# Performance work log

Measured on AMD Instinct MI355X. Metric: run time of the kernel, lower is better.

Reference implementation:

```python
import jax, jax.numpy as jnp
import numpy as np

N, E = 8000, 64000
DNE, DED, DXPD = 128, 128, 64
H, LMAX = 8, 2
S = 1 + 2 * LMAX            # 5 coefficient slots
CD = S * DNE                # coeff_dim = 640
DH = DNE // H               # head dim = 16
CH = CD // H                # coeff head = 80


def _lin(k, din, dout):
    # xavier-ish init for a [din, dout] weight used as x @ W
    return (jax.random.normal(k, (din, dout), jnp.float32) / np.sqrt(din)).astype(jnp.float32)


def _mlp(x, W1, b1, W2, b2):
    # Linear -> SiLU -> (Dropout p, eval) -> Linear
    return jax.nn.silu(x @ W1 + b1) @ W2 + b2


def _seg_sum(x, idx, n):
    return jax.ops.segment_sum(x, idx, num_segments=n)


def _rej(x, r):
    # vector_rejection: remove component of x [E,m,d] parallel to r [E,m]
    r3 = r[:, :, None]
    return x - jnp.sum(x * r3, axis=1, keepdims=True) * r3


def setup_inputs() -> dict:
    key = jax.random.key(0)
    ks = jax.random.split(key, 40)
    inp = {
        "h":  jax.random.normal(ks[0], (N, DNE), jnp.float32),
        "t":  jax.random.normal(ks[1], (E, DED), jnp.float32),
        "X1": jax.random.normal(ks[2], (N, 3, DNE), jnp.float32),
        "X2": jax.random.normal(ks[3], (N, 5, DNE), jnp.float32),
        "r1": jax.random.normal(ks[4], (E, 3), jnp.float32),
        "r2": jax.random.normal(ks[5], (E, 5), jnp.float32),
        "c":  jax.random.uniform(ks[6], (E, 1), jnp.float32),
        "edge": jax.random.randint(ks[7], (E, 2), 0, N, jnp.int32),
    }
    # GATA params
    inp["Wq"], inp["bq"] = _lin(ks[8], DNE, DNE), jnp.zeros((DNE,), jnp.float32)
    inp["Wk"], inp["bk"] = _lin(ks[9], DNE, DNE), jnp.zeros((DNE,), jnp.float32)
    inp["Wre"], inp["bre"] = _lin(ks[10], DED, DNE), jnp.zeros((DNE,), jnp.float32)
    inp["Wv1"], inp["bv1"] = _lin(ks[11], DNE, DNE), jnp.zeros((DNE,), jnp.float32)
    inp["Wv2"], inp["bv2"] = _lin(ks[12], DNE, CD), jnp.zeros((CD,), jnp.float32)
    inp["Wrs"], inp["brs"] = _lin(ks[13], DED, CD), jnp.zeros((CD,), jnp.float32)
    inp["Ws1"], inp["bs1"] = _lin(ks[14], DNE, DNE), jnp.zeros((DNE,), jnp.float32)
    inp["Ws2"], inp["bs2"] = _lin(ks[15], DNE, CD), jnp.zeros((CD,), jnp.float32)
    # HTR params
    inp["Wvq"] = _lin(ks[16], DNE, DXPD)
    inp["Wvk1"] = _lin(ks[17], DNE, DXPD)
    inp["Wvk2"] = _lin(ks[18], DNE, DXPD)
    inp["Ww1"], inp["bw1"] = _lin(ks[19], DXPD, DXPD), jnp.zeros((DXPD,), jnp.float32)
    inp["Ww2"], inp["bw2"] = _lin(ks[20], DXPD, DED), jnp.zeros((DED,), jnp.float32)
    inp["Wt1"], inp["bt1"] = _lin(ks[21], DED, DED), jnp.zeros((DED,), jnp.float32)
    inp["Wt2"], inp["bt2"] = _lin(ks[22], DED, DED), jnp.zeros((DED,), jnp.float32)
    return inp


def reference(h, t, X1, X2, r1, r2, c, edge,
              Wq, bq, Wk, bk, Wre, bre, Wv1, bv1, Wv2, bv2,
              Wrs, brs, Ws1, bs1, Ws2, bs2,
              Wvq, Wvk1, Wvk2, Ww1, bw1, Ww2, bw2, Wt1, bt1, Wt2, bt2):
    i, j = edge[:, 0], edge[:, 1]
    # multi-head attention logits over edges
    q = (h[i] @ Wq + bq).reshape(E, H, DH)
    k = (h[j] @ Wk + bk).reshape(E, H, DH)
    geom = jax.nn.silu(t @ Wre + bre).reshape(E, H, DH)
    alpha = jnp.sum(q * (k * geom), axis=-1)                       # [E,H]
    # segment softmax over destination node i
    mx = jnp.full((N, H), -jnp.inf, jnp.float32).at[i].max(alpha)
    mx = jnp.maximum(mx, -1e9)
    ex = jnp.exp(alpha - mx[i])
    den = jnp.maximum(_seg_sum(ex, i, N), 1e-12)
    attn = ex / den[i]
    deg = jnp.zeros((N,), jnp.float32).at[i].add(1.0)              # bincount
    attn = attn * (jnp.sqrt(deg[i]) / np.sqrt(DNE))[:, None]       # [E,H]
    # values + spatial branch
    v = _mlp(h[j], Wv1, bv1, Wv2, bv2).reshape(E, H, CH)
    sea = attn[:, :, None] * v
    tp = (t @ Wrs + brs).reshape(E, H, CH)
    s = _mlp(h[j], Ws1, bs1, Ws2, bs2).reshape(E, H, CH)
    spatial = tp * s * c[:, None, :]
    coeff = (sea + spatial).reshape(E, S, DNE)
    # scalar update
    h_out = h + _seg_sum(coeff[:, 0, :], i, N)
    # steerable updates (l = 1, 2)
    Xl, rl, X_out = [X1, X2], [r1, r2], []
    for l in (1, 2):
        o_d = coeff[:, l, :]          # direction coeff
        o_t = coeff[:, LMAX + l, :]   # tensor coeff
        msg = rl[l - 1][:, :, None] * o_d[:, None, :] + Xl[l - 1][j] * o_t[:, None, :]
        X_out.append(Xl[l - 1] + _seg_sum(msg, i, N))
    # HTR edge refinement
    Xcat = jnp.concatenate(X_out, axis=1)                          # [N,8,dne]
    Q = (Xcat @ Wvq)[i]                                            # [E,8,dxpd]
    K = jnp.concatenate([X_out[0] @ Wvk1, X_out[1] @ Wvk2], axis=1)[j]
    Q = jnp.concatenate([_rej(Q[:, :3], r1), _rej(Q[:, 3:], r2)], axis=1)
    K = jnp.concatenate([_rej(K[:, :3], -r1), _rej(K[:, 3:], -r2)], axis=1)
    w = jnp.sum(Q * K, axis=1)                                     # [E,dxpd]
    t_out = t + _mlp(w, Ww1, bw1, Ww2, bw2) * _mlp(t, Wt1, bt1, Wt2, bt2)
    return (h_out, t_out, X_out[0], X_out[1])
```

## Files before the change

kernel.cpp:

```cpp
#include <hip/hip_runtime.h>
#include <cstdint>
#include <cmath>

#define NN 8000
#define NE 64000
#define DNE 128
#define NHD 8
#define CDIM 640

typedef unsigned short u16;
typedef u16   u16x8 __attribute__((ext_vector_type(8)));
typedef __bf16 v8bf __attribute__((ext_vector_type(8)));
typedef float  v4f  __attribute__((ext_vector_type(4)));

static __device__ __forceinline__ u16 f2bf(float f) {
    unsigned int u = __float_as_uint(f);
    u += 0x7FFF + ((u >> 16) & 1);
    return (u16)(u >> 16);
}
static __device__ __forceinline__ float bf2f(u16 v) {
    return __uint_as_float(((unsigned int)v) << 16);
}

constexpr size_t O_TBF   = 0;
constexpr size_t O_X1BF  = O_TBF   + 16384000;
constexpr size_t O_X2BF  = O_X1BF  + 6160384;
constexpr size_t O_X1OBF = O_X2BF  + 10256384;
constexpr size_t O_X2OBF = O_X1OBF + 6160384;
constexpr size_t O_WARE  = O_X2OBF + 10256384;
constexpr size_t O_CNT   = O_WARE  + 811008;
constexpr size_t O_CURS  = O_CNT   + 32000;
constexpr size_t O_OFFS  = O_CURS  + 32000;
constexpr size_t O_EIDS  = O_OFFS  + 32768;
constexpr size_t O_HV    = O_EIDS  + 256000;
constexpr size_t O_HS    = O_HV    + 10321920;
constexpr size_t O_ATTN  = O_HS    + 10321920;
constexpr size_t O_TEMP  = O_ATTN  + 2048000;
constexpr size_t O_GEOM  = O_TEMP;
constexpr size_t O_HQ    = O_GEOM + 16384000;
constexpr size_t O_HK    = O_HQ   + 2064384;
constexpr size_t O_VMID  = O_HK   + 2064384;
constexpr size_t O_SMID  = O_VMID + 2064384;
constexpr size_t O_ALPHA = O_SMID + 2064384;
constexpr size_t O_COEFF = O_TEMP;
constexpr size_t O_Q1K1  = O_TEMP;
constexpr size_t O_Q2K2  = O_Q1K1 + 6160384;
constexpr size_t O_WBUF  = O_Q2K2 + 10256384;
constexpr size_t O_WMID  = O_WBUF + 8192000;
constexpr size_t O_WOUT  = O_WMID + 8192000;
constexpr size_t O_TMID  = O_WOUT + 16384000;

__device__ const int WOFFA[14] = {0,16384,32768,49152,65536,81920,98304,114688,196608,278528,360448,364544,372736,389120};

struct WTArgs { const float* w[16]; };
__global__ void wtrans_all(WTArgs a, u16* __restrict__ ob) {
    int s = blockIdx.y;
    int id = blockIdx.x * 256 + threadIdx.x;
    if (s < 12) {
        int K = (s < 10) ? 128 : 64;
        int N = (s < 7) ? 128 : ((s < 10) ? 640 : ((s == 10) ? 64 : 128));
        if (id >= K * N) return;
        int k = id / N, n = id % N;
        ob[WOFFA[s] + (size_t)n * K + k] = f2bf(a.w[s][id]);
    } else {
        if (id >= 16384) return;
        int n = id >> 7, k = id & 127;
        const float* wa = a.w[s == 12 ? 12 : 14];
        const float* wb = a.w[s == 12 ? 13 : 15];
        ob[WOFFA[s] + id] = f2bf(n < 64 ? wa[k * 64 + n] : wb[k * 64 + (n - 64)]);
    }
}

struct ConvArgs { const float* in[4]; u16* out[4]; };
__global__ void conv_all(ConvArgs a) {
    int s = blockIdx.y;
    int padr = (s == 0) ? 8064 : ((s == 1) ? 64000 : ((s == 2) ? 24064 : 40064));
    int realr = (s == 0) ? 8000 : ((s == 1) ? 64000 : ((s == 2) ? 24000 : 40000));
    int id4 = (blockIdx.x * 256 + threadIdx.x) * 4;
    if (id4 >= padr * 128) return;
    int row = id4 >> 7;
    float4 v = make_float4(0.f, 0.f, 0.f, 0.f);
    if (row < realr) v = *(const float4*)(a.in[s] + id4);
    u16* o = a.out[s] + id4;
    o[0] = f2bf(v.x); o[1] = f2bf(v.y); o[2] = f2bf(v.z); o[3] = f2bf(v.w);
}

template<int BN, int WROWS, int WCOLS, int MODE>
__global__ __launch_bounds__(256) void mm_bf16(
    const u16* __restrict__ A, const u16* __restrict__ Bt,
    const float* __restrict__ bias, void* __restrict__ out,
    int Ncols, int K, int act,
    const int* __restrict__ edge, const float* __restrict__ attn,
    const u16* __restrict__ hv, const u16* __restrict__ hs,
    const float* __restrict__ cvals,
    const float* __restrict__ tresid, const u16* __restrict__ wmul)
{
    constexpr int BM = 128, BK = 32, LDA = 40;
    constexpr int MT = BM / WROWS / 16;
    constexpr int NT = BN / WCOLS / 16;
    __shared__ u16 sA[BM * LDA];
    __shared__ u16 sB[BN * LDA];
    const int tid = threadIdx.x;
    const int wave = tid >> 6, lane = tid & 63;
    const int lane15 = lane & 15, quad = lane >> 4;
    const int wm = wave / WCOLS, wn = wave % WCOLS;
    const int row0 = blockIdx.y * BM, col0 = blockIdx.x * BN;
    const int arow = wm * (BM / WROWS);
    const int brow = wn * (BN / WCOLS);
    v4f acc[MT][NT] = {};
    for (int k0 = 0; k0 < K; k0 += BK) {
        #pragma unroll
        for (int ci = 0; ci < (BM * BK / 8) / 256; ++ci) {
            int cch = tid + ci * 256;
            int m = cch >> 2, ko = (cch & 3) * 8;
            u16x8 v = *(const u16x8*)(A + (size_t)(row0 + m) * K + k0 + ko);
            *(u16x8*)(&sA[m * LDA + ko]) = v;
        }
        #pragma unroll
        for (int ci = 0; ci < (BN * BK / 8) / 256; ++ci) {
            int cch = tid + ci * 256;
            int n = cch >> 2, ko = (cch & 3) * 8;
            u16x8 v = *(const u16x8*)(Bt + (size_t)(col0 + n) * K + k0 + ko);
            *(u16x8*)(&sB[n * LDA + ko]) = v;
        }
        __syncthreads();
        v8bf af[MT], bfr[NT];
        #pragma unroll
        for (int mt = 0; mt < MT; ++mt)
            af[mt] = __builtin_bit_cast(v8bf, *(const u16x8*)(&sA[(arow + mt * 16 + lane15) * LDA + quad * 8]));
        #pragma unroll
        for (int nt = 0; nt < NT; ++nt)
            bfr[nt] = __builtin_bit_cast(v8bf, *(const u16x8*)(&sB[(brow + nt * 16 + lane15) * LDA + quad * 8]));
        #pragma unroll
        for (int mt = 0; mt < MT; ++mt)
            #pragma unroll
            for (int nt = 0; nt < NT; ++nt)
                acc[mt][nt] = __builtin_amdgcn_mfma_f32_16x16x32_bf16(af[mt], bfr[nt], acc[mt][nt], 0, 0, 0);
        __syncthreads();
    }
    #pragma unroll
    for (int mt = 0; mt < MT; ++mt) {
        #pragma unroll
        for (int r = 0; r < 4; ++r) {
            int grow = row0 + arow + mt * 16 + quad * 4 + r;
            if (MODE == 2) {
                int e = grow;
                int jn = edge[2 * e + 1];
                float ce = cvals[e];
                const u16* hvr = hv + (size_t)jn * CDIM;
                const u16* hsr = hs + (size_t)jn * CDIM;
                u16* orow = (u16*)out + (size_t)e * CDIM;
                #pragma unroll
                for (int nt = 0; nt < NT; ++nt) {
                    int gcol = col0 + brow + nt * 16 + lane15;
                    float tp = acc[mt][nt][r] + bias[gcol];
                    float at = attn[e * NHD + gcol / 80];
                    float v = at * bf2f(hvr[gcol]) + tp * bf2f(hsr[gcol]) * ce;
                    orow[gcol] = f2bf(v);
                }
            } else if (MODE == 3) {
                size_t base = (size_t)grow * Ncols;
                #pragma unroll
                for (int nt = 0; nt < NT; ++nt) {
                    int gcol = col0 + brow + nt * 16 + lane15;
                    float v = acc[mt][nt][r] + bias[gcol];
                    ((float*)out)[base + gcol] = tresid[base + gcol] + bf2f(wmul[base + gcol]) * v;
                }
            } else {
                u16* orow = (u16*)out + (size_t)grow * Ncols;
                #pragma unroll
                for (int nt = 0; nt < NT; ++nt) {
                    int gcol = col0 + brow + nt * 16 + lane15;
                    float v = acc[mt][nt][r];
                    if (bias) v += bias[gcol];
                    if (act) v = v / (1.0f + expf(-v));
                    orow[gcol] = f2bf(v);
                }
            }
        }
    }
}

__global__ void zero_i32_kernel(int* a, int n) {
    int t = blockIdx.x * 256 + threadIdx.x;
    if (t < n) a[t] = 0;
}
__global__ void count_kernel(const int* __restrict__ edge, int* __restrict__ cnt, int E_) {
    int e = blockIdx.x * 256 + threadIdx.x;
    if (e < E_) atomicAdd(&cnt[edge[2 * e]], 1);
}
__global__ __launch_bounds__(1024) void scan_kernel(const int* __restrict__ cnt, int* __restrict__ offs, int n) {
    __shared__ int s[1024];
    int t = threadIdx.x;
    int base = t * 8;
    int loc[8];
    int sum = 0;
    #pragma unroll
    for (int q = 0; q < 8; ++q) {
        int idx = base + q;
        int v = (idx < n) ? cnt[idx] : 0;
        loc[q] = v; sum += v;
    }
    s[t] = sum;
    __syncthreads();
    for (int off = 1; off < 1024; off <<= 1) {
        int v = (t >= off) ? s[t - off] : 0;
        __syncthreads();
        s[t] += v;
        __syncthreads();
    }
    int run = s[t] - sum;
    #pragma unroll
    for (int q = 0; q < 8; ++q) {
        int idx = base + q;
        if (idx < n) offs[idx] = run;
        run += loc[q];
    }
    if (t == 1023) offs[n] = s[1023];
}
__global__ void fill_kernel(const int* __restrict__ edge, const int* __restrict__ offs,
                            int* __restrict__ cursor, int* __restrict__ eids, int E_) {
    int e = blockIdx.x * 256 + threadIdx.x;
    if (e >= E_) return;
    int i = edge[2 * e];
    int pos = atomicAdd(&cursor[i], 1);
    eids[offs[i] + pos] = e;
}

__global__ __launch_bounds__(256) void alpha_kernel(
    const u16* __restrict__ hq, const u16* __restrict__ hk, const u16* __restrict__ geom,
    const int* __restrict__ edge, float* __restrict__ alpha)
{
    int e = blockIdx.x * 2 + (threadIdx.x >> 7);
    int d = threadIdx.x & 127;
    int i = edge[2 * e], j = edge[2 * e + 1];
    float p = bf2f(hq[(size_t)i * DNE + d]) * bf2f(hk[(size_t)j * DNE + d]) * bf2f(geom[(size_t)e * DNE + d]);
    p += __shfl_xor(p, 1);
    p += __shfl_xor(p, 2);
    p += __shfl_xor(p, 4);
    p += __shfl_xor(p, 8);
    if ((d & 15) == 0) alpha[e * NHD + (d >> 4)] = p;
}

__global__ __launch_bounds__(64) void softmax_kernel(
    const float* __restrict__ alpha, const int* __restrict__ offs, const int* __restrict__ eids,
    float* __restrict__ attn)
{
    int node = blockIdx.x;
    int t = threadIdx.x;
    int g = t >> 3, hh = t & 7;
    int beg = offs[node], end = offs[node + 1];
    int deg = end - beg;
    __shared__ float sm[8][8];
    __shared__ float ss[8][8];
    float m = -1e9f;
    for (int p = beg + g; p < end; p += 8) {
        int e = eids[p];
        m = fmaxf(m, alpha[e * NHD + hh]);
    }
    sm[g][hh] = m;
    __syncthreads();
    if (g == 0) {
        float mm = sm[0][hh];
        #pragma unroll
        for (int q = 1; q < 8; ++q) mm = fmaxf(mm, sm[q][hh]);
        sm[0][hh] = mm;
    }
    __syncthreads();
    float mx = sm[0][hh];
    float ssum = 0.f;
    for (int p = beg + g; p < end; p += 8) {
        int e = eids[p];
        ssum += expf(alpha[e * NHD + hh] - mx);
    }
    ss[g][hh] = ssum;
    __syncthreads();
    if (g == 0) {
        float tot = 0.f;
        #pragma unroll
        for (int q = 0; q < 8; ++q) tot += ss[q][hh];
        ss[0][hh] = fmaxf(tot, 1e-12f);
    }
    __syncthreads();
    float den = ss[0][hh];
    float scale = sqrtf((float)deg) * 0.08838834764831845f;
    for (int p = beg + g; p < end; p += 8) {
        int e = eids[p];
        attn[e * NHD + hh] = expf(alpha[e * NHD + hh] - mx) / den * scale;
    }
}

__global__ __launch_bounds__(128) void scatter_kernel(
    const u16* __restrict__ coeff, const int* __restrict__ edge,
    const float* __restrict__ r1, const float* __restrict__ r2,
    const float* __restrict__ h, const float* __restrict__ X1, const float* __restrict__ X2,
    const u16* __restrict__ X1bf, const u16* __restrict__ X2bf,
    const int* __restrict__ offs, const int* __restrict__ eids,
    float* __restrict__ h_out, float* __restrict__ X1_out, float* __restrict__ X2_out,
    u16* __restrict__ X1obf, u16* __restrict__ X2obf)
{
    int n = blockIdx.x;
    int d = threadIdx.x;
    int beg = offs[n], end = offs[n + 1];
    float hacc = 0.f;
    float x1a[3] = {0.f, 0.f, 0.f};
    float x2a[5] = {0.f, 0.f, 0.f, 0.f, 0.f};
    for (int p = beg; p < end; ++p) {
        int e = eids[p];
        int j = edge[2 * e + 1];
        const u16* crow = coeff + (size_t)e * CDIM;
        float c0  = bf2f(crow[d]);
        float od1 = bf2f(crow[128 + d]);
        float od2 = bf2f(crow[256 + d]);
        float ot1 = bf2f(crow[384 + d]);
        float ot2 = bf2f(crow[512 + d]);
        hacc += c0;
        #pragma unroll
        for (int a = 0; a < 3; ++a)
            x1a[a] += r1[e * 3 + a] * od1 + bf2f(X1bf[((size_t)j * 3 + a) * DNE + d]) * ot1;
        #pragma unroll
        for (int a = 0; a < 5; ++a)
            x2a[a] += r2[e * 5 + a] * od2 + bf2f(X2bf[((size_t)j * 5 + a) * DNE + d]) * ot2;
    }
    h_out[(size_t)n * DNE + d] = h[(size_t)n * DNE + d] + hacc;
    #pragma unroll
    for (int a = 0; a < 3; ++a) {
        size_t idx = ((size_t)n * 3 + a) * DNE + d;
        float v = X1[idx] + x1a[a];
        X1_out[idx] = v;
        X1obf[idx] = f2bf(v);
    }
    #pragma unroll
    for (int a = 0; a < 5; ++a) {
        size_t idx = ((size_t)n * 5 + a) * DNE + d;
        float v = X2[idx] + x2a[a];
        X2_out[idx] = v;
        X2obf[idx] = f2bf(v);
    }
}

__global__ __launch_bounds__(256) void w_kernel(
    const u16* __restrict__ QK1, const u16* __restrict__ QK2,
    const int* __restrict__ edge, const float* __restrict__ r1, const float* __restrict__ r2,
    u16* __restrict__ w, int E_)
{
    int e = blockIdx.x * 4 + (threadIdx.x >> 6);
    int d = threadIdx.x & 63;
    if (e >= E_) return;
    int i = edge[2 * e], j = edge[2 * e + 1];
    float q[8], k[8];
    #pragma unroll
    for (int a = 0; a < 3; ++a) {
        q[a] = bf2f(QK1[((size_t)i * 3 + a) * 128 + d]);
        k[a] = bf2f(QK1[((size_t)j * 3 + a) * 128 + 64 + d]);
    }
    #pragma unroll
    for (int a = 0; a < 5; ++a) {
        q[3 + a] = bf2f(QK2[((size_t)i * 5 + a) * 128 + d]);
        k[3 + a] = bf2f(QK2[((size_t)j * 5 + a) * 128 + 64 + d]);
    }
    float ra[3], rb[5];
    #pragma unroll
    for (int a = 0; a < 3; ++a) ra[a] = r1[e * 3 + a];
    #pragma unroll
    for (int a = 0; a < 5; ++a) rb[a] = r2[e * 5 + a];
    float dq1 = 0.f, dk1 = 0.f, dq2 = 0.f, dk2 = 0.f;
    #pragma unroll
    for (int a = 0; a < 3; ++a) { dq1 += q[a] * ra[a]; dk1 += k[a] * ra[a]; }
    #pragma unroll
    for (int a = 0; a < 5; ++a) { dq2 += q[3 + a] * rb[a]; dk2 += k[3 + a] * rb[a]; }
    float acc = 0.f;
    #pragma unroll
    for (int a = 0; a < 3; ++a) acc += (q[a] - dq1 * ra[a]) * (k[a] - dk1 * ra[a]);
    #pragma unroll
    for (int a = 0; a < 5; ++a) acc += (q[3 + a] - dq2 * rb[a]) * (k[3 + a] - dk2 * rb[a]);
    w[(size_t)e * 64 + d] = f2bf(acc);
}

extern "C" void kernel_launch(void* const* d_in, const int* in_sizes, int n_in,
                              void* d_out, int out_size, void* d_ws, size_t ws_size,
                              hipStream_t stream)
{
    const float* h    = (const float*)d_in[0];
    const float* t    = (const float*)d_in[1];
    const float* X1   = (const float*)d_in[2];
    const float* X2   = (const float*)d_in[3];
    const float* r1   = (const float*)d_in[4];
    const float* r2   = (const float*)d_in[5];
    const float* c    = (const float*)d_in[6];
    const int*   edge = (const int*)d_in[7];
    const float* Wq   = (const float*)d_in[8];  const float* bq  = (const float*)d_in[9];
    const float* Wk   = (const float*)d_in[10]; const float* bk  = (const float*)d_in[11];
    const float* Wre  = (const float*)d_in[12]; const float* bre = (const float*)d_in[13];
    const float* Wv1  = (const float*)d_in[14]; const float* bv1 = (const float*)d_in[15];
    const float* Wv2  = (const float*)d_in[16]; const float* bv2 = (const float*)d_in[17];
    const float* Wrs  = (const float*)d_in[18]; const float* brs = (const float*)d_in[19];
    const float* Ws1  = (const float*)d_in[20]; const float* bs1 = (const float*)d_in[21];
    const float* Ws2  = (const float*)d_in[22]; const float* bs2 = (const float*)d_in[23];
    const float* Wvq  = (const float*)d_in[24];
    const float* Wvk1 = (const float*)d_in[25];
    const float* Wvk2 = (const float*)d_in[26];
    const float* Ww1  = (const float*)d_in[27]; const float* bw1 = (const float*)d_in[28];
    const float* Ww2  = (const float*)d_in[29]; const float* bw2 = (const float*)d_in[30];
    const float* Wt1  = (const float*)d_in[31]; const float* bt1 = (const float*)d_in[32];
    const float* Wt2  = (const float*)d_in[33]; const float* bt2 = (const float*)d_in[34];

    char* ws = (char*)d_ws;
    float* h_out  = (float*)d_out;
    float* t_out  = h_out + (size_t)NN * DNE;
    float* X1_out = t_out + (size_t)NE * 128;
    float* X2_out = X1_out + (size_t)NN * 3 * DNE;

    u16* t_bf   = (u16*)(ws + O_TBF);
    u16* X1bf   = (u16*)(ws + O_X1BF);
    u16* X2bf   = (u16*)(ws + O_X2BF);
    u16* X1obf  = (u16*)(ws + O_X1OBF);
    u16* X2obf  = (u16*)(ws + O_X2OBF);
    u16* ware   = (u16*)(ws + O_WARE);
    int* cnt    = (int*)(ws + O_CNT);
    int* cursor = (int*)(ws + O_CURS);
    int* offs   = (int*)(ws + O_OFFS);
    int* eids   = (int*)(ws + O_EIDS);
    u16* hv_bf  = (u16*)(ws + O_HV);
    u16* hs_bf  = (u16*)(ws + O_HS);
    float* attn = (float*)(ws + O_ATTN);
    u16* geom   = (u16*)(ws + O_GEOM);
    u16* hq     = (u16*)(ws + O_HQ);
    u16* hk     = (u16*)(ws + O_HK);
    u16* vmid   = (u16*)(ws + O_VMID);
    u16* smid   = (u16*)(ws + O_SMID);
    float* alpha= (float*)(ws + O_ALPHA);
    u16* coeff  = (u16*)(ws + O_COEFF);
    u16* Q1K1   = (u16*)(ws + O_Q1K1);
    u16* Q2K2   = (u16*)(ws + O_Q2K2);
    u16* wbuf   = (u16*)(ws + O_WBUF);
    u16* wmid   = (u16*)(ws + O_WMID);
    u16* wout   = (u16*)(ws + O_WOUT);
    u16* tmid   = (u16*)(ws + O_TMID);

    u16* WqT  = ware + 0;      u16* WkT  = ware + 16384;  u16* WreT = ware + 32768;
    u16* Wv1T = ware + 49152;  u16* Ws1T = ware + 65536;  u16* Wt1T = ware + 81920;
    u16* Wt2T = ware + 98304;  u16* Wv2T = ware + 114688; u16* WrsT = ware + 196608;
    u16* Ws2T = ware + 278528; u16* Ww1T = ware + 360448; u16* Ww2T = ware + 364544;
    u16* WA1T = ware + 372736; u16* WA2T = ware + 389120;

    WTArgs wt;
    wt.w[0] = Wq;  wt.w[1] = Wk;  wt.w[2] = Wre; wt.w[3] = Wv1; wt.w[4] = Ws1;
    wt.w[5] = Wt1; wt.w[6] = Wt2; wt.w[7] = Wv2; wt.w[8] = Wrs; wt.w[9] = Ws2;
    wt.w[10] = Ww1; wt.w[11] = Ww2; wt.w[12] = Wvq; wt.w[13] = Wvk1; wt.w[14] = Wvq; wt.w[15] = Wvk2;
    wtrans_all<<<dim3(320, 14), 256, 0, stream>>>(wt, ware);

    ConvArgs ca;
    ca.in[0] = h;  ca.out[0] = hq;
    ca.in[0] = h;    ca.out[0] = (u16*)(ws + O_HQ);
    u16* h_bf = (u16*)(ws + O_ALPHA);
    h_bf = (u16*)(ws + O_TMID + 16384000);
    ca.in[0] = h;  ca.out[0] = h_bf;
    ca.in[1] = t;  ca.out[1] = t_bf;
    ca.in[2] = X1; ca.out[2] = X1bf;
    ca.in[3] = X2; ca.out[3] = X2bf;
    conv_all<<<dim3(8000, 4), 256, 0, stream>>>(ca);

    zero_i32_kernel<<<63, 256, 0, stream>>>(cnt, 16000);
    count_kernel<<<250, 256, 0, stream>>>(edge, cnt, NE);
    scan_kernel<<<1, 1024, 0, stream>>>(cnt, offs, NN);
    fill_kernel<<<250, 256, 0, stream>>>(edge, offs, cursor, eids, NE);

    const int* np = nullptr; const float* nf = nullptr; const u16* nu = nullptr;
    #define MMSTD(A_, B_, bias_, out_, NC_, K_, act_, gy_) \
        mm_bf16<128,2,2,0><<<dim3((NC_)/128, gy_), 256, 0, stream>>>((A_), (B_), (bias_), (out_), (NC_), (K_), (act_), np, nf, nu, nu, nf, nf, nu)

    MMSTD(h_bf, WqT,  bq,  hq,   128, 128, 0, 63);
    MMSTD(h_bf, WkT,  bk,  hk,   128, 128, 0, 63);
    MMSTD(h_bf, Wv1T, bv1, vmid, 128, 128, 1, 63);
    MMSTD(vmid, Wv2T, bv2, hv_bf, 640, 128, 0, 63);
    MMSTD(h_bf, Ws1T, bs1, smid, 128, 128, 1, 63);
    MMSTD(smid, Ws2T, bs2, hs_bf, 640, 128, 0, 63);
    MMSTD(t_bf, WreT, bre, geom, 128, 128, 1, 500);

    alpha_kernel<<<NE / 2, 256, 0, stream>>>(hq, hk, geom, edge, alpha);
    softmax_kernel<<<NN, 64, 0, stream>>>(alpha, offs, eids, attn);

    mm_bf16<128,2,2,2><<<dim3(5, 500), 256, 0, stream>>>(
        t_bf, WrsT, brs, coeff, 640, 128, 0, edge, attn, hv_bf, hs_bf, c, nf, nu);

    scatter_kernel<<<NN, 128, 0, stream>>>(coeff, edge, r1, r2, h, X1, X2, X1bf, X2bf,
                                           offs, eids, h_out, X1_out, X2_out, X1obf, X2obf);

    MMSTD(X1obf, WA1T, nullptr, Q1K1, 128, 128, 0, 188);
    MMSTD(X2obf, WA2T, nullptr, Q2K2, 128, 128, 0, 313);

    w_kernel<<<NE / 4, 256, 0, stream>>>(Q1K1, Q2K2, edge, r1, r2, wbuf, NE);

    mm_bf16<64,4,1,0><<<dim3(1, 500), 256, 0, stream>>>(
        wbuf, Ww1T, bw1, wmid, 64, 64, 1, np, nf, nu, nu, nf, nf, nu);
    MMSTD(wmid, Ww2T, bw2, wout, 128, 64, 0, 500);
    MMSTD(t_bf, Wt1T, bt1, tmid, 128, 128, 1, 500);
    mm_bf16<128,2,2,3><<<dim3(1, 500), 256, 0, stream>>>(
        tmid, Wt2T, bt2, t_out, 128, 128, 0, np, nf, nu, nu, nf, t, wout);
}
```

Measured before the change: 585.5 us.

## Fuse node projections, alpha into geom GEMM, and chain edge MLPs

Concatenates the Wq/Wk/Wv1/Ws1 projections into one 512-wide GEMM with a per-column SiLU, and folds the alpha dot product into the epilogue of the geometric GEMM, which removes the separate alpha kernel and the geom buffer. The w-MLP and t-MLP two-layer chains each become a single kernel that keeps the hidden activation in shared memory instead of writing it to global. This removes several launches and intermediate global round-trips, at the cost of heavier epilogues with gathers and larger shared-memory use per block.

```diff
diff --git a/kernel.cpp b/kernel.cpp
--- a/kernel.cpp
+++ b/kernel.cpp
@@ -23,7 +23,7 @@
 }
 
 constexpr size_t O_TBF   = 0;
-constexpr size_t O_X1BF  = O_TBF   + 16384000;
+constexpr size_t O_X1BF  = 16384000;
 constexpr size_t O_X2BF  = O_X1BF  + 6160384;
 constexpr size_t O_X1OBF = O_X2BF  + 10256384;
 constexpr size_t O_X2OBF = O_X1OBF + 6160384;
@@ -35,25 +35,21 @@
 constexpr size_t O_HV    = O_EIDS  + 256000;
 constexpr size_t O_HS    = O_HV    + 10321920;
 constexpr size_t O_ATTN  = O_HS    + 10321920;
-constexpr size_t O_TEMP  = O_ATTN  + 2048000;
-constexpr size_t O_GEOM  = O_TEMP;
-constexpr size_t O_HQ    = O_GEOM + 16384000;
-constexpr size_t O_HK    = O_HQ   + 2064384;
-constexpr size_t O_VMID  = O_HK   + 2064384;
-constexpr size_t O_SMID  = O_VMID + 2064384;
-constexpr size_t O_ALPHA = O_SMID + 2064384;
+constexpr size_t O_B512  = O_ATTN  + 2048000;
+constexpr size_t O_TEMP  = O_B512  + 2048;
+constexpr size_t O_QKVS  = O_TEMP;
+constexpr size_t O_ALPHA = O_QKVS + 8257536;
+constexpr size_t O_HBF   = O_ALPHA + 2048000;
 constexpr size_t O_COEFF = O_TEMP;
 constexpr size_t O_Q1K1  = O_TEMP;
 constexpr size_t O_Q2K2  = O_Q1K1 + 6160384;
 constexpr size_t O_WBUF  = O_Q2K2 + 10256384;
-constexpr size_t O_WMID  = O_WBUF + 8192000;
-constexpr size_t O_WOUT  = O_WMID + 8192000;
-constexpr size_t O_TMID  = O_WOUT + 16384000;
+constexpr size_t O_WOUT  = O_WBUF + 8192000;
 
 __device__ const int WOFFA[14] = {0,16384,32768,49152,65536,81920,98304,114688,196608,278528,360448,364544,372736,389120};
 
-struct WTArgs { const float* w[16]; };
-__global__ void wtrans_all(WTArgs a, u16* __restrict__ ob) {
+struct WTArgs { const float* w[16]; const float* b[4]; };
+__global__ void wtrans_all(WTArgs a, u16* __restrict__ ob, float* __restrict__ bias512) {
     int s = blockIdx.y;
     int id = blockIdx.x * 256 + threadIdx.x;
     if (s < 12) {
@@ -62,12 +58,15 @@
         if (id >= K * N) return;
         int k = id / N, n = id % N;
         ob[WOFFA[s] + (size_t)n * K + k] = f2bf(a.w[s][id]);
-    } else {
+    } else if (s < 14) {
         if (id >= 16384) return;
         int n = id >> 7, k = id & 127;
         const float* wa = a.w[s == 12 ? 12 : 14];
         const float* wb = a.w[s == 12 ? 13 : 15];
         ob[WOFFA[s] + id] = f2bf(n < 64 ? wa[k * 64 + n] : wb[k * 64 + (n - 64)]);
+    } else {
+        if (id >= 512) return;
+        bias512[id] = a.b[id >> 7][id & 127];
     }
 }
 
@@ -85,43 +84,38 @@
     o[0] = f2bf(v.x); o[1] = f2bf(v.y); o[2] = f2bf(v.z); o[3] = f2bf(v.w);
 }
 
-template<int BN, int WROWS, int WCOLS, int MODE>
+template<int MODE>
 __global__ __launch_bounds__(256) void mm_bf16(
-    const u16* __restrict__ A, const u16* __restrict__ Bt,
+    const u16* __restrict__ A, int As, const u16* __restrict__ Bt,
     const float* __restrict__ bias, void* __restrict__ out,
     int Ncols, int K, int act,
     const int* __restrict__ edge, const float* __restrict__ attn,
     const u16* __restrict__ hv, const u16* __restrict__ hs,
-    const float* __restrict__ cvals,
-    const float* __restrict__ tresid, const u16* __restrict__ wmul)
+    const float* __restrict__ cvals)
 {
-    constexpr int BM = 128, BK = 32, LDA = 40;
-    constexpr int MT = BM / WROWS / 16;
-    constexpr int NT = BN / WCOLS / 16;
+    constexpr int BM = 128, BN = 128, BK = 32, LDA = 40;
+    constexpr int MT = 4, NT = 4;
     __shared__ u16 sA[BM * LDA];
     __shared__ u16 sB[BN * LDA];
     const int tid = threadIdx.x;
     const int wave = tid >> 6, lane = tid & 63;
     const int lane15 = lane & 15, quad = lane >> 4;
-    const int wm = wave / WCOLS, wn = wave % WCOLS;
+    const int wm = wave >> 1, wn = wave & 1;
     const int row0 = blockIdx.y * BM, col0 = blockIdx.x * BN;
-    const int arow = wm * (BM / WROWS);
-    const int brow = wn * (BN / WCOLS);
+    const int arow = wm * 64, brow = wn * 64;
     v4f acc[MT][NT] = {};
     for (int k0 = 0; k0 < K; k0 += BK) {
         #pragma unroll
-        for (int ci = 0; ci < (BM * BK / 8) / 256; ++ci) {
+        for (int ci = 0; ci < 2; ++ci) {
             int cch = tid + ci * 256;
             int m = cch >> 2, ko = (cch & 3) * 8;
-            u16x8 v = *(const u16x8*)(A + (size_t)(row0 + m) * K + k0 + ko);
-            *(u16x8*)(&sA[m * LDA + ko]) = v;
-        }
-        #pragma unroll
-        for (int ci = 0; ci < (BN * BK / 8) / 256; ++ci) {
+            *(u16x8*)(&sA[m * LDA + ko]) = *(const u16x8*)(A + (size_t)(row0 + m) * As + k0 + ko);
+        }
+        #pragma unroll
+        for (int ci = 0; ci < 2; ++ci) {
             int cch = tid + ci * 256;
             int n = cch >> 2, ko = (cch & 3) * 8;
-            u16x8 v = *(const u16x8*)(Bt + (size_t)(col0 + n) * K + k0 + ko);
-            *(u16x8*)(&sB[n * LDA + ko]) = v;
+            *(u16x8*)(&sB[n * LDA + ko]) = *(const u16x8*)(Bt + (size_t)(col0 + n) * K + k0 + ko);
         }
         __syncthreads();
         v8bf af[MT], bfr[NT];
@@ -158,13 +152,23 @@
                     float v = at * bf2f(hvr[gcol]) + tp * bf2f(hsr[gcol]) * ce;
                     orow[gcol] = f2bf(v);
                 }
-            } else if (MODE == 3) {
-                size_t base = (size_t)grow * Ncols;
+            } else if (MODE == 4) {
+                int e = grow;
+                int i2 = edge[2 * e], j2 = edge[2 * e + 1];
+                const u16* qb = hv + (size_t)i2 * 512;
+                const u16* kb = hv + (size_t)j2 * 512 + 128;
                 #pragma unroll
                 for (int nt = 0; nt < NT; ++nt) {
                     int gcol = col0 + brow + nt * 16 + lane15;
-                    float v = acc[mt][nt][r] + bias[gcol];
-                    ((float*)out)[base + gcol] = tresid[base + gcol] + bf2f(wmul[base + gcol]) * v;
+                    float g = acc[mt][nt][r] + bias[gcol];
+                    g = g / (1.0f + expf(-g));
+                    float p = g * bf2f(qb[gcol]) * bf2f(kb[gcol]);
+                    p += __shfl_xor(p, 1);
+                    p += __shfl_xor(p, 2);
+                    p += __shfl_xor(p, 4);
+                    p += __shfl_xor(p, 8);
+                    if (lane15 == 0)
+                        ((float*)out)[(size_t)e * NHD + ((col0 + brow) >> 4) + nt] = p;
                 }
             } else {
                 u16* orow = (u16*)out + (size_t)grow * Ncols;
@@ -173,12 +177,212 @@
                     int gcol = col0 + brow + nt * 16 + lane15;
                     float v = acc[mt][nt][r];
                     if (bias) v += bias[gcol];
-                    if (act) v = v / (1.0f + expf(-v));
+                    if (act == 1 || (act == 2 && gcol >= 256)) v = v / (1.0f + expf(-v));
                     orow[gcol] = f2bf(v);
                 }
             }
         }
     }
+}
+
+__global__ __launch_bounds__(256) void wchain_kernel(
+    const u16* __restrict__ wbuf, const u16* __restrict__ W1T, const u16* __restrict__ W2T,
+    const float* __restrict__ b1, const float* __restrict__ b2, u16* __restrict__ wout)
+{
+    __shared__ u16 sw[128 * 72];
+    __shared__ u16 sm[128 * 72];
+    __shared__ u16 sW1[64 * 72];
+    __shared__ u16 sW2[128 * 72];
+    const int tid = threadIdx.x;
+    const int wave = tid >> 6, lane = tid & 63;
+    const int lane15 = lane & 15, quad = lane >> 4;
+    const int row0 = blockIdx.x * 128;
+    #pragma unroll
+    for (int ci = 0; ci < 4; ++ci) {
+        int cch = tid + ci * 256;
+        int m = cch >> 3, ko = (cch & 7) * 8;
+        *(u16x8*)(&sw[m * 72 + ko]) = *(const u16x8*)(wbuf + (size_t)(row0 + m) * 64 + ko);
+    }
+    #pragma unroll
+    for (int ci = 0; ci < 2; ++ci) {
+        int cch = tid + ci * 256;
+        int n = cch >> 3, ko = (cch & 7) * 8;
+        *(u16x8*)(&sW1[n * 72 + ko]) = *(const u16x8*)(W1T + (size_t)n * 64 + ko);
+    }
+    #pragma unroll
+    for (int ci = 0; ci < 4; ++ci) {
+        int cch = tid + ci * 256;
+        int n = cch >> 3, ko = (cch & 7) * 8;
+        *(u16x8*)(&sW2[n * 72 + ko]) = *(const u16x8*)(W2T + (size_t)n * 64 + ko);
+    }
+    __syncthreads();
+    v4f a1[2][4] = {};
+    #pragma unroll
+    for (int kk = 0; kk < 2; ++kk) {
+        int k0 = kk * 32;
+        v8bf af[2], bfr[4];
+        #pragma unroll
+        for (int mt = 0; mt < 2; ++mt)
+            af[mt] = __builtin_bit_cast(v8bf, *(const u16x8*)(&sw[(wave * 32 + mt * 16 + lane15) * 72 + k0 + quad * 8]));
+        #pragma unroll
+        for (int nt = 0; nt < 4; ++nt)
+            bfr[nt] = __builtin_bit_cast(v8bf, *(const u16x8*)(&sW1[(nt * 16 + lane15) * 72 + k0 + quad * 8]));
+        #pragma unroll
+        for (int mt = 0; mt < 2; ++mt)
+            #pragma unroll
+            for (int nt = 0; nt < 4; ++nt)
+                a1[mt][nt] = __builtin_amdgcn_mfma_f32_16x16x32_bf16(af[mt], bfr[nt], a1[mt][nt], 0, 0, 0);
+    }
+    #pragma unroll
+    for (int mt = 0; mt < 2; ++mt)
+        #pragma unroll
+        for (int r = 0; r < 4; ++r) {
+            int mrow = wave * 32 + mt * 16 + quad * 4 + r;
+            #pragma unroll
+            for (int nt = 0; nt < 4; ++nt) {
+                int mcol = nt * 16 + lane15;
+                float v = a1[mt][nt][r] + b1[mcol];
+                v = v / (1.0f + expf(-v));
+                sm[mrow * 72 + mcol] = f2bf(v);
+            }
+        }
+    __syncthreads();
+    const int wm = wave >> 1, wn = wave & 1;
+    const int arow = wm * 64, brow = wn * 64;
+    v4f a2[4][4] = {};
+    #pragma unroll
+    for (int kk = 0; kk < 2; ++kk) {
+        int k0 = kk * 32;
+        v8bf af[4], bfr[4];
+        #pragma unroll
+        for (int mt = 0; mt < 4; ++mt)
+            af[mt] = __builtin_bit_cast(v8bf, *(const u16x8*)(&sm[(arow + mt * 16 + lane15) * 72 + k0 + quad * 8]));
+        #pragma unroll
+        for (int nt = 0; nt < 4; ++nt)
+            bfr[nt] = __builtin_bit_cast(v8bf, *(const u16x8*)(&sW2[(brow + nt * 16 + lane15) * 72 + k0 + quad * 8]));
+        #pragma unroll
+        for (int mt = 0; mt < 4; ++mt)
+            #pragma unroll
+            for (int nt = 0; nt < 4; ++nt)
+                a2[mt][nt] = __builtin_amdgcn_mfma_f32_16x16x32_bf16(af[mt], bfr[nt], a2[mt][nt], 0, 0, 0);
+    }
+    #pragma unroll
+    for (int mt = 0; mt < 4; ++mt)
+        #pragma unroll
+        for (int r = 0; r < 4; ++r) {
+            int grow = row0 + arow + mt * 16 + quad * 4 + r;
+            #pragma unroll
+            for (int nt = 0; nt < 4; ++nt) {
+                int gcol = brow + nt * 16 + lane15;
+                wout[(size_t)grow * 128 + gcol] = f2bf(a2[mt][nt][r] + b2[gcol]);
+            }
+        }
+}
+
+__global__ __launch_bounds__(256) void tchain_kernel(
+    const u16* __restrict__ tbf, const u16* __restrict__ W1T, const u16* __restrict__ W2T,
+    const float* __restrict__ b1, const float* __restrict__ b2,
+    const float* __restrict__ tin, const u16* __restrict__ wout,
+    float* __restrict__ t_out)
+{
+    constexpr int LDA = 136;
+    __shared__ u16 sA[128 * LDA];
+    __shared__ u16 sW[128 * 72];
+    const int tid = threadIdx.x;
+    const int wave = tid >> 6, lane = tid & 63;
+    const int lane15 = lane & 15, quad = lane >> 4;
+    const int wm = wave >> 1, wn = wave & 1;
+    const int arow = wm * 64, brow = wn * 64;
+    const int row0 = blockIdx.x * 128;
+    #pragma unroll
+    for (int ci = 0; ci < 8; ++ci) {
+        int cch = tid + ci * 256;
+        int m = cch >> 4, ko = (cch & 15) * 8;
+        *(u16x8*)(&sA[m * LDA + ko]) = *(const u16x8*)(tbf + (size_t)(row0 + m) * 128 + ko);
+    }
+    v4f acc[4][4] = {};
+    #pragma unroll
+    for (int kh = 0; kh < 2; ++kh) {
+        __syncthreads();
+        #pragma unroll
+        for (int ci = 0; ci < 4; ++ci) {
+            int cch = tid + ci * 256;
+            int n = cch >> 3, ko = (cch & 7) * 8;
+            *(u16x8*)(&sW[n * 72 + ko]) = *(const u16x8*)(W1T + (size_t)n * 128 + kh * 64 + ko);
+        }
+        __syncthreads();
+        #pragma unroll
+        for (int kk = 0; kk < 2; ++kk) {
+            int k0 = kh * 64 + kk * 32;
+            v8bf af[4], bfr[4];
+            #pragma unroll
+            for (int mt = 0; mt < 4; ++mt)
+                af[mt] = __builtin_bit_cast(v8bf, *(const u16x8*)(&sA[(arow + mt * 16 + lane15) * LDA + k0 + quad * 8]));
+            #pragma unroll
+            for (int nt = 0; nt < 4; ++nt)
+                bfr[nt] = __builtin_bit_cast(v8bf, *(const u16x8*)(&sW[(brow + nt * 16 + lane15) * 72 + kk * 32 + quad * 8]));
+            #pragma unroll
+            for (int mt = 0; mt < 4; ++mt)
+                #pragma unroll
+                for (int nt = 0; nt < 4; ++nt)
+                    acc[mt][nt] = __builtin_amdgcn_mfma_f32_16x16x32_bf16(af[mt], bfr[nt], acc[mt][nt], 0, 0, 0);
+        }
+    }
+    __syncthreads();
+    #pragma unroll
+    for (int mt = 0; mt < 4; ++mt)
+        #pragma unroll
+        for (int r = 0; r < 4; ++r) {
+            int mrow = arow + mt * 16 + quad * 4 + r;
+            #pragma unroll
+            for (int nt = 0; nt < 4; ++nt) {
+                int mcol = brow + nt * 16 + lane15;
+                float v = acc[mt][nt][r] + b1[mcol];
+                v = v / (1.0f + expf(-v));
+                sA[mrow * LDA + mcol] = f2bf(v);
+            }
+        }
+    v4f acc2[4][4] = {};
+    #pragma unroll
+    for (int kh = 0; kh < 2; ++kh) {
+        __syncthreads();
+        #pragma unroll
+        for (int ci = 0; ci < 4; ++ci) {
+            int cch = tid + ci * 256;
+            int n = cch >> 3, ko = (cch & 7) * 8;
+            *(u16x8*)(&sW[n * 72 + ko]) = *(const u16x8*)(W2T + (size_t)n * 128 + kh * 64 + ko);
+        }
+        __syncthreads();
+        #pragma unroll
+        for (int kk = 0; kk < 2; ++kk) {
+            int k0 = kh * 64 + kk * 32;
+            v8bf af[4], bfr[4];
+            #pragma unroll
+            for (int mt = 0; mt < 4; ++mt)
+                af[mt] = __builtin_bit_cast(v8bf, *(const u16x8*)(&sA[(arow + mt * 16 + lane15) * LDA + k0 + quad * 8]));
+            #pragma unroll
+            for (int nt = 0; nt < 4; ++nt)
+                bfr[nt] = __builtin_bit_cast(v8bf, *(const u16x8*)(&sW[(brow + nt * 16 + lane15) * 72 + kk * 32 + quad * 8]));
+            #pragma unroll
+            for (int mt = 0; mt < 4; ++mt)
+                #pragma unroll
+                for (int nt = 0; nt < 4; ++nt)
+                    acc2[mt][nt] = __builtin_amdgcn_mfma_f32_16x16x32_bf16(af[mt], bfr[nt], acc2[mt][nt], 0, 0, 0);
+        }
+    }
+    #pragma unroll
+    for (int mt = 0; mt < 4; ++mt)
+        #pragma unroll
+        for (int r = 0; r < 4; ++r) {
+            int grow = row0 + arow + mt * 16 + quad * 4 + r;
+            size_t base = (size_t)grow * 128;
+            #pragma unroll
+            for (int nt = 0; nt < 4; ++nt) {
+                int gcol = brow + nt * 16 + lane15;
+                float v = acc2[mt][nt][r] + b2[gcol];
+                t_out[base + gcol] = tin[base + gcol] + bf2f(wout[base + gcol]) * v;
+            }
+        }
 }
 
 __global__ void zero_i32_kernel(int* a, int n) {
@@ -225,21 +429,6 @@
     int i = edge[2 * e];
     int pos = atomicAdd(&cursor[i], 1);
     eids[offs[i] + pos] = e;
-}
-
-__global__ __launch_bounds__(256) void alpha_kernel(
-    const u16* __restrict__ hq, const u16* __restrict__ hk, const u16* __restrict__ geom,
-    const int* __restrict__ edge, float* __restrict__ alpha)
-{
-    int e = blockIdx.x * 2 + (threadIdx.x >> 7);
-    int d = threadIdx.x & 127;
-    int i = edge[2 * e], j = edge[2 * e + 1];
-    float p = bf2f(hq[(size_t)i * DNE + d]) * bf2f(hk[(size_t)j * DNE + d]) * bf2f(geom[(size_t)e * DNE + d]);
-    p += __shfl_xor(p, 1);
-    p += __shfl_xor(p, 2);
-    p += __shfl_xor(p, 4);
-    p += __shfl_xor(p, 8);
-    if ((d & 15) == 0) alpha[e * NHD + (d >> 4)] = p;
 }
 
 __global__ __launch_bounds__(64) void softmax_kernel(
@@ -424,37 +613,36 @@
     u16* hv_bf  = (u16*)(ws + O_HV);
     u16* hs_bf  = (u16*)(ws + O_HS);
     float* attn = (float*)(ws + O_ATTN);
-    u16* geom   = (u16*)(ws + O_GEOM);
-    u16* hq     = (u16*)(ws + O_HQ);
-    u16* hk     = (u16*)(ws + O_HK);
-    u16* vmid   = (u16*)(ws + O_VMID);
-    u16* smid   = (u16*)(ws + O_SMID);
+    float* bias512 = (float*)(ws + O_B512);
+    u16* qkvs   = (u16*)(ws + O_QKVS);
     float* alpha= (float*)(ws + O_ALPHA);
+    u16* h_bf   = (u16*)(ws + O_HBF);
     u16* coeff  = (u16*)(ws + O_COEFF);
     u16* Q1K1   = (u16*)(ws + O_Q1K1);
     u16* Q2K2   = (u16*)(ws + O_Q2K2);
     u16* wbuf   = (u16*)(ws + O_WBUF);
-    u16* wmid   = (u16*)(ws + O_WMID);
     u16* wout   = (u16*)(ws + O_WOUT);
-    u16* tmid   = (u16*)(ws + O_TMID);
-
-    u16* WqT  = ware + 0;      u16* WkT  = ware + 16384;  u16* WreT = ware + 32768;
-    u16* Wv1T = ware + 49152;  u16* Ws1T = ware + 65536;  u16* Wt1T = ware + 81920;
-    u16* Wt2T = ware + 98304;  u16* Wv2T = ware + 114688; u16* WrsT = ware + 196608;
-    u16* Ws2T = ware + 278528; u16* Ww1T = ware + 360448; u16* Ww2T = ware + 364544;
-    u16* WA1T = ware + 372736; u16* WA2T = ware + 389120;
+
+    u16* WqkvsT = ware + 0;
+    u16* WreT = ware + 65536;
+    u16* Wt1T = ware + 81920;
+    u16* Wt2T = ware + 98304;
+    u16* Wv2T = ware + 114688;
+    u16* WrsT = ware + 196608;
+    u16* Ws2T = ware + 278528;
+    u16* Ww1T = ware + 360448;
+    u16* Ww2T = ware + 364544;
+    u16* WA1T = ware + 372736;
+    u16* WA2T = ware + 389120;
 
     WTArgs wt;
-    wt.w[0] = Wq;  wt.w[1] = Wk;  wt.w[2] = Wre; wt.w[3] = Wv1; wt.w[4] = Ws1;
+    wt.w[0] = Wq;  wt.w[1] = Wk;  wt.w[2] = Wv1; wt.w[3] = Ws1; wt.w[4] = Wre;
     wt.w[5] = Wt1; wt.w[6] = Wt2; wt.w[7] = Wv2; wt.w[8] = Wrs; wt.w[9] = Ws2;
     wt.w[10] = Ww1; wt.w[11] = Ww2; wt.w[12] = Wvq; wt.w[13] = Wvk1; wt.w[14] = Wvq; wt.w[15] = Wvk2;
-    wtrans_all<<<dim3(320, 14), 256, 0, stream>>>(wt, ware);
+    wt.b[0] = bq; wt.b[1] = bk; wt.b[2] = bv1; wt.b[3] = bs1;
+    wtrans_all<<<dim3(320, 15), 256, 0, stream>>>(wt, ware, bias512);
 
     ConvArgs ca;
-    ca.in[0] = h;  ca.out[0] = hq;
-    ca.in[0] = h;    ca.out[0] = (u16*)(ws + O_HQ);
-    u16* h_bf = (u16*)(ws + O_ALPHA);
-    h_bf = (u16*)(ws + O_TMID + 16384000);
     ca.in[0] = h;  ca.out[0] = h_bf;
     ca.in[1] = t;  ca.out[1] = t_bf;
     ca.in[2] = X1; ca.out[2] = X1bf;
@@ -467,35 +655,30 @@
     fill_kernel<<<250, 256, 0, stream>>>(edge, offs, cursor, eids, NE);
 
     const int* np = nullptr; const float* nf = nullptr; const u16* nu = nullptr;
-    #define MMSTD(A_, B_, bias_, out_, NC_, K_, act_, gy_) \
-        mm_bf16<128,2,2,0><<<dim3((NC_)/128, gy_), 256, 0, stream>>>((A_), (B_), (bias_), (out_), (NC_), (K_), (act_), np, nf, nu, nu, nf, nf, nu)
-
-    MMSTD(h_bf, WqT,  bq,  hq,   128, 128, 0, 63);
-    MMSTD(h_bf, WkT,  bk,  hk,   128, 128, 0, 63);
-    MMSTD(h_bf, Wv1T, bv1, vmid, 128, 128, 1, 63);
-    MMSTD(vmid, Wv2T, bv2, hv_bf, 640, 128, 0, 63);
-    MMSTD(h_bf, Ws1T, bs1, smid, 128, 128, 1, 63);
-    MMSTD(smid, Ws2T, bs2, hs_bf, 640, 128, 0, 63);
-    MMSTD(t_bf, WreT, bre, geom, 128, 128, 1, 500);
-
-    alpha_kernel<<<NE / 2, 256, 0, stream>>>(hq, hk, geom, edge, alpha);
+
+    mm_bf16<0><<<dim3(4, 63), 256, 0, stream>>>(h_bf, 128, WqkvsT, bias512, qkvs,
+                                                512, 128, 2, np, nf, nu, nu, nf);
+    mm_bf16<0><<<dim3(5, 63), 256, 0, stream>>>(qkvs + 256, 512, Wv2T, bv2, hv_bf,
+                                                640, 128, 0, np, nf, nu, nu, nf);
+    mm_bf16<0><<<dim3(5, 63), 256, 0, stream>>>(qkvs + 384, 512, Ws2T, bs2, hs_bf,
+                                                640, 128, 0, np, nf, nu, nu, nf);
+    mm_bf16<4><<<dim3(1, 500), 256, 0, stream>>>(t_bf, 128, WreT, bre, alpha,
+                                                 128, 128, 0, edge, nf, qkvs, nu, nf);
     softmax_kernel<<<NN, 64, 0, stream>>>(alpha, offs, eids, attn);
 
-    mm_bf16<128,2,2,2><<<dim3(5, 500), 256, 0, stream>>>(
-        t_bf, WrsT, brs, coeff, 640, 128, 0, edge, attn, hv_bf, hs_bf, c, nf, nu);
+    mm_bf16<2><<<dim3(5, 500), 256, 0, stream>>>(t_bf, 128, WrsT, brs, coeff,
+                                                 640, 128, 0, edge, attn, hv_bf, hs_bf, c);
 
     scatter_kernel<<<NN, 128, 0, stream>>>(coeff, edge, r1, r2, h, X1, X2, X1bf, X2bf,
                                            offs, eids, h_out, X1_out, X2_out, X1obf, X2obf);
 
-    MMSTD(X1obf, WA1T, nullptr, Q1K1, 128, 128, 0, 188);
-    MMSTD(X2obf, WA2T, nullptr, Q2K2, 128, 128, 0, 313);
+    mm_bf16<0><<<dim3(1, 188), 256, 0, stream>>>(X1obf, 128, WA1T, nullptr, Q1K1,
+                                                 128, 128, 0, np, nf, nu, nu, nf);
+    mm_bf16<0><<<dim3(1, 313), 256, 0, stream>>>(X2obf, 128, WA2T, nullptr, Q2K2,
+                                                 128, 128, 0, np, nf, nu, nu, nf);
 
     w_kernel<<<NE / 4, 256, 0, stream>>>(Q1K1, Q2K2, edge, r1, r2, wbuf, NE);
 
-    mm_bf16<64,4,1,0><<<dim3(1, 500), 256, 0, stream>>>(
-        wbuf, Ww1T, bw1, wmid, 64, 64, 1, np, nf, nu, nu, nf, nf, nu);
-    MMSTD(wmid, Ww2T, bw2, wout, 128, 64, 0, 500);
-    MMSTD(t_bf, Wt1T, bt1, tmid, 128, 128, 1, 500);
-    mm_bf16<128,2,2,3><<<dim3(1, 500), 256, 0, stream>>>(
-        tmid, Wt2T, bt2, t_out, 128, 128, 0, np, nf, nu, nu, nf, t, wout);
-}
+    wchain_kernel<<<500, 256, 0, stream>>>(wbuf, Ww1T, Ww2T, bw1, bw2, wout);
+    tchain_kernel<<<500, 256, 0, stream>>>(t_bf, Wt1T, Wt2T, bt1, bt2, t, wout, t_out);
+}
```

After: 503.8 us. -14.0%, faster.
